# Kernel tuning notes

Measured on AMD Instinct MI355X. Metric: run time of the kernel, lower is better.

Reference implementation:

```python
import jax, jax.numpy as jnp
import numpy as np

NUM_HEADS = 8
ROPE_BASE = 10000.0


def _rope_cache(T, D, dtype=jnp.float32):
    # LLaMA-style rope cache: cos/sin of shape [T, D]
    inv_freq = 1.0 / (ROPE_BASE ** (jnp.arange(0, D, 2, dtype=dtype) / D))
    t = jnp.arange(T, dtype=dtype)
    freqs = t[:, None] * inv_freq[None, :]            # [T, D/2]
    emb = jnp.concatenate([freqs, freqs], axis=-1)    # [T, D]
    return jnp.cos(emb), jnp.sin(emb)


def _rotate_half(x):
    x1, x2 = jnp.split(x, 2, axis=-1)
    return jnp.concatenate([-x2, x1], axis=-1)


def setup_inputs() -> dict:
    key = jax.random.key(0)
    k1, k2, k3 = jax.random.split(key, 3)
    B, T, C = 4, 2048, 512
    x = jax.random.normal(k1, (B, T, C), dtype=jnp.float32)
    Wqkv = jax.random.normal(k2, (C, 3 * C), dtype=jnp.float32) * (1.0 / np.sqrt(C))
    Wproj = jax.random.normal(k3, (C, C), dtype=jnp.float32) * (1.0 / np.sqrt(C))
    return {"x": x, "Wqkv": Wqkv, "Wproj": Wproj}


def reference(x, Wqkv, Wproj):
    B, T, C = x.shape
    H = NUM_HEADS
    D = C // H

    qkv = jnp.einsum('btc,cf->btf', x, Wqkv)          # [B,T,3C]
    qkv = qkv.reshape(B, T, H, 3 * D)
    q, k, v = jnp.split(qkv, 3, axis=-1)              # each [B,T,H,D]
    q = q.transpose(0, 2, 1, 3)                       # [B,H,T,D]
    k = k.transpose(0, 2, 1, 3)
    v = v.transpose(0, 2, 1, 3)

    cos, sin = _rope_cache(T, D, dtype=x.dtype)       # [T,D]
    cos = cos[None, None, :, :]
    sin = sin[None, None, :, :]
    q = q * cos + _rotate_half(q) * sin
    k = k * cos + _rotate_half(k) * sin

    scale = 1.0 / np.sqrt(D)
    scores = jnp.einsum('bhqd,bhkd->bhqk', q, k) * scale  # [B,H,T,T]
    causal = jnp.tril(jnp.ones((T, T), dtype=bool))
    scores = jnp.where(causal[None, None, :, :], scores, jnp.finfo(scores.dtype).min)
    attn = jax.nn.softmax(scores, axis=-1)
    out = jnp.einsum('bhqk,bhkd->bhqd', attn, v)      # [B,H,T,D]
    out = out.transpose(0, 2, 1, 3).reshape(B, T, C)
    return jnp.einsum('btc,cd->btd', out, Wproj)
```

## Files before the change

### kernel.cpp

```cpp
#include <hip/hip_runtime.h>
#include <hip/hip_bf16.h>
#include <stdint.h>

constexpr int Bn = 4;
constexpr int Tn = 2048;
constexpr int Cn = 512;
constexpr int Hn = 8;
constexpr int Dn = 64;
constexpr int BT = Bn * Tn;
constexpr int NQKV = 3 * Cn;

typedef __attribute__((ext_vector_type(4))) float  f32x4;
typedef __attribute__((ext_vector_type(8))) short  s16x8;
typedef __attribute__((ext_vector_type(4))) short  s16x4;

__device__ __forceinline__ short f2bs(float f) {
    __hip_bfloat16 h = __float2bfloat16(f);
    return *reinterpret_cast<short*>(&h);
}

__device__ __forceinline__ void gload16(const short* g, short* l) {
    __builtin_amdgcn_global_load_lds(
        (const __attribute__((address_space(1))) void*)g,
        (__attribute__((address_space(3))) void*)l, 16, 0, 0);
}


__global__ __launch_bounds__(256) void k_prep(const float* __restrict__ x,
                                              const float* __restrict__ Wqkv,
                                              const float* __restrict__ Wproj,
                                              short* __restrict__ xb,
                                              short* __restrict__ wqkvT,
                                              short* __restrict__ wprojT,
                                              float2* __restrict__ csT) {
    const int bid = blockIdx.x;
    const int tid = threadIdx.x;
    __shared__ float lds[64 * 65];

    if (bid < 4096) {
        int i = bid * 256 + tid;
        f32x4 v = reinterpret_cast<const f32x4*>(x)[i];
        s16x4 o;
        o[0] = f2bs(v[0]); o[1] = f2bs(v[1]); o[2] = f2bs(v[2]); o[3] = f2bs(v[3]);
        reinterpret_cast<s16x4*>(xb)[i] = o;
    } else if (bid < 4352) {
        int wb = bid - 4096;
        const float* W; short* out; int N, n0, k0;
        if (wb < 192) {
            W = Wqkv; out = wqkvT; N = NQKV;
            n0 = (wb >> 3) * 64; k0 = (wb & 7) * 64;
        } else {
            wb -= 192;
            W = Wproj; out = wprojT; N = Cn;
            n0 = (wb >> 3) * 64; k0 = (wb & 7) * 64;
        }
#pragma unroll
        for (int i = 0; i < 16; ++i) {
            int flat = i * 256 + tid;
            int k = flat >> 6, n = flat & 63;
            lds[n * 65 + k] = W[(size_t)(k0 + k) * N + n0 + n];
        }
        __syncthreads();
#pragma unroll
        for (int i = 0; i < 16; ++i) {
            int flat = i * 256 + tid;
            int n = flat >> 6, k = flat & 63;
            out[(size_t)(n0 + n) * 512 + k0 + k] = f2bs(lds[n * 65 + k]);
        }
    } else {
        int i = (bid - 4352) * 256 + tid;
        int t = i >> 6, d = i & 63;
        float inv = exp2f(-(float)(d & 31) * 0.41524101186f);
        float fr = (float)t * inv;
        csT[i] = make_float2(cosf(fr), sinf(fr));
    }
}


template <int MODE>
__global__ __launch_bounds__(256, 2) void gemm_kernel(
    const short* __restrict__ A, const short* __restrict__ Bt,
    const float2* __restrict__ csT,
    short* __restrict__ Qb, short* __restrict__ Kb, short* __restrict__ Vt,
    float* __restrict__ outF) {
    const int m0 = blockIdx.y * 128;
    const int n0 = blockIdx.x * 128;
    const int tid = threadIdx.x;
    const int w = tid >> 6, lane = tid & 63;
    const int qi = lane & 15, g = lane >> 4;
    const int wr = w >> 1, wc = w & 1;

    __shared__ short As[2][128 * 64];
    __shared__ short Bs[2][128 * 64];

    f32x4 acc[4][4];
#pragma unroll
    for (int mt = 0; mt < 4; ++mt)
#pragma unroll
        for (int nt = 0; nt < 4; ++nt) acc[mt][nt] = (f32x4){0.f, 0.f, 0.f, 0.f};

    const int lr = lane >> 3;
    const int lc = (lane & 7) ^ lr;

#define STAGEG(buf, k0)                                                         \
    {                                                                           \
        _Pragma("unroll")                                                       \
        for (int s4_ = 0; s4_ < 4; ++s4_) {                                     \
            int slot_ = s4_ * 4 + w;                                            \
            int r_ = slot_ * 8 + lr;                                            \
            gload16(&A[(size_t)(m0 + r_) * 512 + (k0) + lc * 8],                \
                    &As[buf][slot_ * 512 + lane * 8]);                          \
            gload16(&Bt[(size_t)(n0 + r_) * 512 + (k0) + lc * 8],               \
                    &Bs[buf][slot_ * 512 + lane * 8]);                          \
        }                                                                       \
    }

    STAGEG(0, 0);
    __syncthreads();

    for (int it = 0; it < 8; ++it) {
        if (it + 1 < 8) STAGEG((it + 1) & 1, (it + 1) * 64);
        const int cur = it & 1;
#pragma unroll
        for (int kk = 0; kk < 2; ++kk) {
            s16x8 af[4], bf[4];
#pragma unroll
            for (int mt = 0; mt < 4; ++mt) {
                int row = wr * 64 + mt * 16 + qi;
                af[mt] = *(const s16x8*)&As[cur][row * 64 + (((kk << 2) | g) ^ (qi & 7)) * 8];
            }
#pragma unroll
            for (int nt = 0; nt < 4; ++nt) {
                int row = wc * 64 + nt * 16 + qi;
                bf[nt] = *(const s16x8*)&Bs[cur][row * 64 + (((kk << 2) | g) ^ (qi & 7)) * 8];
            }
#pragma unroll
            for (int mt = 0; mt < 4; ++mt)
#pragma unroll
                for (int nt = 0; nt < 4; ++nt)
                    acc[mt][nt] = __builtin_amdgcn_mfma_f32_16x16x32_bf16(
                        af[mt], bf[nt], acc[mt][nt], 0, 0, 0);
        }
        __syncthreads();
    }
#undef STAGEG

    if (MODE == 1) {
#pragma unroll
        for (int mt = 0; mt < 4; ++mt)
#pragma unroll
            for (int nt = 0; nt < 4; ++nt)
#pragma unroll
                for (int r = 0; r < 4; ++r)
                    outF[(size_t)(m0 + wr * 64 + mt * 16 + 4 * g + r) * 512 +
                         n0 + wc * 64 + nt * 16 + qi] = acc[mt][nt][r];
    } else {
        const int seg64 = (n0 >> 6) + wc;
        const int h = seg64 / 3;
        const int seg = seg64 % 3;
        const int b = m0 >> 11;
        const int tb = (m0 & 2047) + wr * 64;
        const float QSC = 0.125f * 1.44269504f;
        if (seg == 2) {
            const size_t vbase = (size_t)(b * Hn + h) * Dn;
#pragma unroll
            for (int mt = 0; mt < 4; ++mt)
#pragma unroll
                for (int nt = 0; nt < 4; ++nt)
#pragma unroll
                    for (int r = 0; r < 4; ++r) {
                        int t = tb + mt * 16 + 4 * g + r;
                        int d = nt * 16 + qi;
                        int o = t & 31;
                        int jj = (t & ~31) + ((o >> 2) & 3) * 8 + (o >> 4) * 4 + (o & 3);
                        Vt[(vbase + d) * Tn + jj] = f2bs(acc[mt][nt][r]);
                    }
        } else {
            short* dst = (seg == 0) ? Qb : Kb;
            const float post = (seg == 0) ? QSC : 1.0f;
            const size_t headbase = (size_t)(b * Hn + h) * Tn;
#pragma unroll
            for (int mt = 0; mt < 4; ++mt)
#pragma unroll
                for (int nt = 0; nt < 4; ++nt)
#pragma unroll
                    for (int r = 0; r < 4; ++r) {
                        int t = tb + mt * 16 + 4 * g + r;
                        int d = nt * 16 + qi;
                        float val = acc[mt][nt][r];
                        float pv = (nt < 2) ? -acc[mt][nt + 2][r] : acc[mt][nt - 2][r];
                        float2 cs = csT[t * 64 + d];
                        dst[(headbase + t) * Dn + d] = f2bs((val * cs.x + pv * cs.y) * post);
                    }
        }
    }
}


__global__ __launch_bounds__(512, 4) void attn_kernel(const short* __restrict__ Qb,
                                                      const short* __restrict__ Kb,
                                                      const short* __restrict__ Vt,
                                                      short* __restrict__ AO) {
    const int idx = blockIdx.x;
    const int bh = idx & 31;
    const int qt = 31 - (idx >> 5);
    const int q0 = qt * 64;
    const int tid = threadIdx.x;
    const int w = tid >> 6, lane = tid & 63;
    const int qi = lane & 15, g = lane >> 4;
    const int grp = w >> 2;
    const int wg = w & 3;
    const int b = bh >> 3, h = bh & 7;

    __shared__ short Ks[2][2][64 * 64];
    __shared__ short Vs[2][2][64 * 64];

    const short* Qh = Qb + (size_t)bh * Tn * Dn;
    const short* Kh = Kb + (size_t)bh * Tn * Dn;
    const short* Vh = Vt + (size_t)bh * Dn * Tn;

    const int wrow0 = q0 + wg * 16;
    s16x8 qf[2];
#pragma unroll
    for (int dh = 0; dh < 2; ++dh)
        qf[dh] = *(const s16x8*)&Qh[(size_t)(wrow0 + qi) * Dn + dh * 32 + g * 8];

    f32x4 O[4];
#pragma unroll
    for (int dt = 0; dt < 4; ++dt) O[dt] = (f32x4){0.f, 0.f, 0.f, 0.f};
    float lsum = 0.f;

    const int nch = qt + 1;
    const int mid = (nch + 1) >> 1;
    const int chbase = grp ? mid : 0;
    const int nmy = grp ? (nch - mid) : mid;
    const f32x4 z4 = {0.f, 0.f, 0.f, 0.f};

    const int lr = lane >> 3;
    const int lc = (lane & 7) ^ lr;

#define STAGE(buf, ch)                                                          \
    {                                                                           \
        const int kv0_ = (ch) * 64;                                             \
        _Pragma("unroll")                                                       \
        for (int i_ = 0; i_ < 2; ++i_) {                                        \
            int slot_ = i_ * 4 + wg;                                            \
            int r_ = slot_ * 8 + lr;                                            \
            gload16(&Kh[(size_t)(kv0_ + r_) * 64 + lc * 8],                     \
                    &Ks[grp][buf][slot_ * 512 + lane * 8]);                     \
            gload16(&Vh[(size_t)r_ * Tn + kv0_ + lc * 8],                       \
                    &Vs[grp][buf][slot_ * 512 + lane * 8]);                     \
        }                                                                       \
    }

    if (nmy > 0) STAGE(0, chbase);

    for (int i = 0; i < mid; ++i) {
        const bool valid = i < nmy;
        const int ch = chbase + i;
        const int kv0 = ch * 64;
        const int cur = i & 1;
        if (valid) {
            if (i + 1 < nmy) {
                STAGE((i + 1) & 1, ch + 1);
                asm volatile("s_waitcnt vmcnt(4)" ::: "memory");
            } else {
                asm volatile("s_waitcnt vmcnt(0)" ::: "memory");
            }
        }
        __builtin_amdgcn_s_barrier();
        asm volatile("" ::: "memory");

        if (valid) {
            f32x4 sacc[4];
            __builtin_amdgcn_s_setprio(1);
#pragma unroll
            for (int sub = 0; sub < 4; ++sub) {
                const int krow = sub * 16 + qi;
                s16x8 ka = *(const s16x8*)&Ks[grp][cur][krow * 64 + ((g ^ (qi & 7))) * 8];
                s16x8 kc = *(const s16x8*)&Ks[grp][cur][krow * 64 + (((4 | g) ^ (qi & 7))) * 8];
                f32x4 t0 = __builtin_amdgcn_mfma_f32_16x16x32_bf16(ka, qf[0], z4, 0, 0, 0);
                sacc[sub] = __builtin_amdgcn_mfma_f32_16x16x32_bf16(kc, qf[1], t0, 0, 0, 0);
            }
            __builtin_amdgcn_s_setprio(0);

            float pe[16];
            if (kv0 + 63 <= wrow0) {
#pragma unroll
                for (int e2 = 0; e2 < 16; ++e2)
                    pe[e2] = exp2f(sacc[e2 >> 2][e2 & 3]);
            } else {
                const int qrow = wrow0 + qi;
#pragma unroll
                for (int sub = 0; sub < 4; ++sub)
#pragma unroll
                    for (int r = 0; r < 4; ++r) {
                        int key = kv0 + sub * 16 + 4 * g + r;
                        pe[sub * 4 + r] = (key <= qrow) ? exp2f(sacc[sub][r]) : 0.f;
                    }
            }
            {
                float a0 = (pe[0] + pe[1]) + (pe[2] + pe[3]);
                float a1 = (pe[4] + pe[5]) + (pe[6] + pe[7]);
                float a2 = (pe[8] + pe[9]) + (pe[10] + pe[11]);
                float a3 = (pe[12] + pe[13]) + (pe[14] + pe[15]);
                lsum += (a0 + a1) + (a2 + a3);
            }
            s16x8 pf[2];
#pragma unroll
            for (int c = 0; c < 2; ++c)
#pragma unroll
                for (int e2 = 0; e2 < 8; ++e2) pf[c][e2] = f2bs(pe[c * 8 + e2]);

            __builtin_amdgcn_s_setprio(1);
#pragma unroll
            for (int c = 0; c < 2; ++c)
#pragma unroll
                for (int dt = 0; dt < 4; ++dt) {
                    const int vrow = dt * 16 + qi;
                    s16x8 vf = *(const s16x8*)&Vs[grp][cur][vrow * 64 +
                                                   ((((c << 2) | g) ^ (qi & 7))) * 8];
                    O[dt] = __builtin_amdgcn_mfma_f32_16x16x32_bf16(
                        pf[c], vf, O[dt], 0, 0, 0);
                }
            __builtin_amdgcn_s_setprio(0);
        }
        asm volatile("" ::: "memory");
        __builtin_amdgcn_s_barrier();
        asm volatile("" ::: "memory");
    }
#undef STAGE

    lsum += __shfl_xor(lsum, 16);
    lsum += __shfl_xor(lsum, 32);

    f32x4* Osc = (f32x4*)&Ks[0][0][0];
    float* Lsc = (float*)&Vs[0][0][0];
    __syncthreads();
    if (grp == 1) {
#pragma unroll
        for (int dt = 0; dt < 4; ++dt)
            Osc[(dt * 4 + wg) * 64 + lane] = O[dt];
        if (g == 0) Lsc[wg * 16 + qi] = lsum;
    }
    __syncthreads();
    if (grp == 0) {
        float lt = lsum + Lsc[wg * 16 + qi];
#pragma unroll
        for (int dt = 0; dt < 4; ++dt) {
            f32x4 p = Osc[(dt * 4 + wg) * 64 + lane];
            O[dt][0] += p[0]; O[dt][1] += p[1]; O[dt][2] += p[2]; O[dt][3] += p[3];
        }
#pragma unroll
        for (int r = 0; r < 4; ++r) {
            float li = __shfl(lt, 4 * g + r);
            float inv = 1.f / li;
            int t = wrow0 + 4 * g + r;
#pragma unroll
            for (int dt = 0; dt < 4; ++dt)
                AO[((size_t)(b * Tn + t)) * Cn + h * 64 + dt * 16 + qi] =
                    f2bs(O[dt][r] * inv);
        }
    }
}


extern "C" void kernel_launch(void* const* d_in, const int* in_sizes, int n_in,
                              void* d_out, int out_size, void* d_ws, size_t ws_size,
                              hipStream_t stream) {
    const float* x = (const float*)d_in[0];
    const float* Wqkv = (const float*)d_in[1];
    const float* Wproj = (const float*)d_in[2];
    float* out = (float*)d_out;

    char* ws = (char*)d_ws;
    size_t o = 0;
    short* xb = (short*)(ws + o);      o += (size_t)BT * Cn * 2;
    short* wqkvT = (short*)(ws + o);   o += (size_t)NQKV * Cn * 2;
    short* wprojT = (short*)(ws + o);  o += (size_t)Cn * Cn * 2;
    short* Qb = (short*)(ws + o);      o += (size_t)Bn * Hn * Tn * Dn * 2;
    short* Kb = (short*)(ws + o);      o += (size_t)Bn * Hn * Tn * Dn * 2;
    short* Vt = (short*)(ws + o);      o += (size_t)Bn * Hn * Tn * Dn * 2;
    float2* csT = (float2*)(ws + o);   o += (size_t)Tn * Dn * 8;

    k_prep<<<dim3(4864), 256, 0, stream>>>(x, Wqkv, Wproj, xb, wqkvT, wprojT, csT);

    gemm_kernel<0><<<dim3(NQKV / 128, BT / 128), 256, 0, stream>>>(
        xb, wqkvT, csT, Qb, Kb, Vt, nullptr);

    attn_kernel<<<dim3(1024), 512, 0, stream>>>(Qb, Kb, Vt, xb );

    gemm_kernel<1><<<dim3(Cn / 128, BT / 128), 256, 0, stream>>>(
        xb , wprojT, csT, nullptr, nullptr, nullptr, out);
}
```

Before: 87.23 us.

## Halve GEMM K-tile to 32, raise occupancy, use explicit vmcnt waits

Shrinks the GEMM K-step from 64 to 32, halving shared memory per block, and raises launch bounds to allow 4 blocks per CU. It rewrites the LDS swizzle for 32-wide rows. It replaces __syncthreads with raw s_barrier plus explicit s_waitcnt vmcnt so the next tile's async load stays in flight during compute. This doubles the number of barrier iterations, and the tighter register budget may cause spills given 64 accumulator floats per thread.

Result: faster. 80.87 us, median of 2 (-7.3%).

```diff
diff --git a/kernel.cpp b/kernel.cpp
--- a/kernel.cpp
+++ b/kernel.cpp
@@ -78,7 +78,7 @@
 
 
 template <int MODE>
-__global__ __launch_bounds__(256, 2) void gemm_kernel(
+__global__ __launch_bounds__(256, 4) void gemm_kernel(
     const short* __restrict__ A, const short* __restrict__ Bt,
     const float2* __restrict__ csT,
     short* __restrict__ Qb, short* __restrict__ Kb, short* __restrict__ Vt,
@@ -90,8 +90,8 @@
     const int qi = lane & 15, g = lane >> 4;
     const int wr = w >> 1, wc = w & 1;
 
-    __shared__ short As[2][128 * 64];
-    __shared__ short Bs[2][128 * 64];
+    __shared__ short As[2][128 * 32];
+    __shared__ short Bs[2][128 * 32];
 
     f32x4 acc[4][4];
 #pragma unroll
@@ -99,49 +99,58 @@
 #pragma unroll
         for (int nt = 0; nt < 4; ++nt) acc[mt][nt] = (f32x4){0.f, 0.f, 0.f, 0.f};
 
-    const int lr = lane >> 3;
-    const int lc = (lane & 7) ^ lr;
+    const int lrr = lane >> 2;
+    const int lp = lane & 3;
 
 #define STAGEG(buf, k0)                                                         \
     {                                                                           \
         _Pragma("unroll")                                                       \
-        for (int s4_ = 0; s4_ < 4; ++s4_) {                                     \
-            int slot_ = s4_ * 4 + w;                                            \
-            int r_ = slot_ * 8 + lr;                                            \
-            gload16(&A[(size_t)(m0 + r_) * 512 + (k0) + lc * 8],                \
-                    &As[buf][slot_ * 512 + lane * 8]);                          \
-            gload16(&Bt[(size_t)(n0 + r_) * 512 + (k0) + lc * 8],               \
-                    &Bs[buf][slot_ * 512 + lane * 8]);                          \
+        for (int i_ = 0; i_ < 2; ++i_) {                                        \
+            int row_ = i_ * 64 + w * 16 + lrr;                                  \
+            int c_ = lp ^ ((row_ ^ (row_ >> 2)) & 3);                           \
+            gload16(&A[(size_t)(m0 + row_) * 512 + (k0) + c_ * 8],              \
+                    &As[buf][(i_ * 64 + w * 16) * 32 + lane * 8]);              \
+            gload16(&Bt[(size_t)(n0 + row_) * 512 + (k0) + c_ * 8],             \
+                    &Bs[buf][(i_ * 64 + w * 16) * 32 + lane * 8]);              \
         }                                                                       \
     }
 
     STAGEG(0, 0);
-    __syncthreads();
-
-    for (int it = 0; it < 8; ++it) {
-        if (it + 1 < 8) STAGEG((it + 1) & 1, (it + 1) * 64);
+
+    for (int it = 0; it < 16; ++it) {
         const int cur = it & 1;
-#pragma unroll
-        for (int kk = 0; kk < 2; ++kk) {
-            s16x8 af[4], bf[4];
-#pragma unroll
-            for (int mt = 0; mt < 4; ++mt) {
-                int row = wr * 64 + mt * 16 + qi;
-                af[mt] = *(const s16x8*)&As[cur][row * 64 + (((kk << 2) | g) ^ (qi & 7)) * 8];
-            }
-#pragma unroll
-            for (int nt = 0; nt < 4; ++nt) {
-                int row = wc * 64 + nt * 16 + qi;
-                bf[nt] = *(const s16x8*)&Bs[cur][row * 64 + (((kk << 2) | g) ^ (qi & 7)) * 8];
-            }
-#pragma unroll
-            for (int mt = 0; mt < 4; ++mt)
-#pragma unroll
-                for (int nt = 0; nt < 4; ++nt)
-                    acc[mt][nt] = __builtin_amdgcn_mfma_f32_16x16x32_bf16(
-                        af[mt], bf[nt], acc[mt][nt], 0, 0, 0);
-        }
-        __syncthreads();
+        if (it + 1 < 16) {
+            STAGEG((it + 1) & 1, (it + 1) * 32);
+            asm volatile("s_waitcnt vmcnt(4)" ::: "memory");
+        } else {
+            asm volatile("s_waitcnt vmcnt(0)" ::: "memory");
+        }
+        __builtin_amdgcn_s_barrier();
+        asm volatile("" ::: "memory");
+
+        s16x8 af[4], bf[4];
+#pragma unroll
+        for (int mt = 0; mt < 4; ++mt) {
+            int row = wr * 64 + mt * 16 + qi;
+            int p = g ^ ((row ^ (row >> 2)) & 3);
+            af[mt] = *(const s16x8*)&As[cur][row * 32 + p * 8];
+        }
+#pragma unroll
+        for (int nt = 0; nt < 4; ++nt) {
+            int row = wc * 64 + nt * 16 + qi;
+            int p = g ^ ((row ^ (row >> 2)) & 3);
+            bf[nt] = *(const s16x8*)&Bs[cur][row * 32 + p * 8];
+        }
+#pragma unroll
+        for (int mt = 0; mt < 4; ++mt)
+#pragma unroll
+            for (int nt = 0; nt < 4; ++nt)
+                acc[mt][nt] = __builtin_amdgcn_mfma_f32_16x16x32_bf16(
+                    af[mt], bf[nt], acc[mt][nt], 0, 0, 0);
+
+        asm volatile("" ::: "memory");
+        __builtin_amdgcn_s_barrier();
+        asm volatile("" ::: "memory");
     }
 #undef STAGEG
 
```
